# Kernel tuning notes

Measured on AMD Instinct MI355X. Metric: run time of the kernel, lower is better.

The kernel has to match this reference:

```python
import jax, jax.numpy as jnp
import numpy as np

N = 100000          # nodes
E = 1600000         # edges (avg degree 16)
H = 128             # hidden_dim
P = 10              # INVARIANT_PHYSICS_DIM
TOTAL = P + H
LN_EPS = 1e-5       # torch LayerNorm default


def setup_inputs() -> dict:
    key = jax.random.key(0)
    ks = jax.random.split(key, 16)
    s = 0.02
    return {
        "physics_x": jax.random.normal(ks[0], (N, P), dtype=jnp.float32),
        "learnable_emb": jax.random.normal(ks[1], (N, H), dtype=jnp.float32),
        "edge_index": jax.random.randint(ks[2], (2, E), 0, N, dtype=jnp.int32),
        "Wq": jax.random.normal(ks[3], (TOTAL, H), dtype=jnp.float32) * s,
        "bq": jnp.zeros((H,), dtype=jnp.float32),
        "Wk": jax.random.normal(ks[4], (TOTAL, H), dtype=jnp.float32) * s,
        "bk": jnp.zeros((H,), dtype=jnp.float32),
        "Wv": jax.random.normal(ks[5], (H, H), dtype=jnp.float32) * s,
        "bv": jnp.zeros((H,), dtype=jnp.float32),
        "Wo": jax.random.normal(ks[6], (H, H), dtype=jnp.float32) * s,
        "bo": jnp.zeros((H,), dtype=jnp.float32),
        "gamma": jnp.ones((H,), dtype=jnp.float32),
        "beta": jnp.zeros((H,), dtype=jnp.float32),
    }


def reference(physics_x, learnable_emb, edge_index, Wq, bq, Wk, bk, Wv, bv, Wo, bo, gamma, beta):
    n_nodes = learnable_emb.shape[0]
    scale = 1.0 / np.sqrt(Wq.shape[1]).astype(np.float32)

    full_repr = jnp.concatenate([physics_x, learnable_emb], axis=-1)   # [N, P+H]
    Q = full_repr @ Wq + bq                                            # [N, H]
    K = full_repr @ Wk + bk                                            # [N, H]
    V = learnable_emb @ Wv + bv                                        # [N, H]

    src, dst = edge_index[0], edge_index[1]
    # per-edge unnormalized attention (NOTE: no max-subtraction, faithful to source)
    attn_scores = jnp.sum(Q[dst] * K[src], axis=-1) * scale            # [E]
    exp_scores = jnp.exp(attn_scores)                                  # [E]
    denom = jax.ops.segment_sum(exp_scores, dst, num_segments=n_nodes) # [N]
    attn_probs = exp_scores / (denom[dst] + 1e-8)                      # [E]

    msg = V[src] * attn_probs[:, None]                                 # [E, H]
    agg = jax.ops.segment_sum(msg, dst, num_segments=n_nodes)          # [N, H]

    out = agg @ Wo + bo
    x = learnable_emb + out
    mu = jnp.mean(x, axis=-1, keepdims=True)
    var = jnp.var(x, axis=-1, keepdims=True)
    return gamma * (x - mu) / jnp.sqrt(var + LN_EPS) + beta
```

## Files before the change

kernel.cpp:

```cpp
#include <hip/hip_runtime.h>
#include <hip/hip_bf16.h>
#include <math.h>

#define PDIM 10
#define HDIM 128
#define TDIM 138
#define AROW 168
#define B_LEN (5 * 8 * 64 * 8)
#define TROW 136

#define CW_WQ 0
#define CW_WK 17664
#define CW_WV 35328
#define CW_WO 51712
#define CW_BQ 68096
#define CW_BK 68224
#define CW_BV 68352
#define CW_BO 68480
#define CW_GA 68608
#define CW_BE 68736
#define CW_TOTAL 68864

typedef short v8s __attribute__((ext_vector_type(8)));
typedef float v4f __attribute__((ext_vector_type(4)));
typedef float v2f __attribute__((ext_vector_type(2)));

#if defined(__has_builtin)
#if __has_builtin(__builtin_amdgcn_cvt_pk_f32_fp8) && __has_builtin(__builtin_amdgcn_cvt_pk_fp8_f32)
#define HAVE_FP8_CVT 1
#endif
#endif
#ifndef HAVE_FP8_CVT
#define HAVE_FP8_CVT 0
#endif

__device__ __forceinline__ float b2f_lo(unsigned u) { return __uint_as_float(u << 16); }
__device__ __forceinline__ float b2f_hi(unsigned u) { return __uint_as_float(u & 0xffff0000u); }
__device__ __forceinline__ unsigned short f2b(float f) {
    unsigned u = __float_as_uint(f);
    u += 0x7fffu + ((u >> 16) & 1u);
    return (unsigned short)(u >> 16);
}

__device__ __forceinline__ float f8_dec1(unsigned b) {
    unsigned e = (b >> 3) & 0xf, m = b & 7;
    float v = e ? __uint_as_float(((e + 120) << 23) | (m << 20))
                : (float)m * 0.001953125f;
    return (b & 0x80) ? -v : v;
}
__device__ __forceinline__ unsigned f8_enc1(float f) {
    unsigned u = __float_as_uint(f);
    unsigned s = (u >> 31) << 7;
    float a = fabsf(f);
    if (a < 0.0009765625f) return s;
    if (a < 0.015625f) {
        int m = (int)(a * 512.f + 0.5f); if (m > 7) m = 7;
        return s | (unsigned)m;
    }
    if (a >= 448.f) return s | 0x7e;
    int ex = (int)((u >> 23) & 0xff);
    unsigned mant = u & 0x7fffff;
    unsigned r = mant >> 20, rem = mant & 0xfffff;
    if (rem > 0x80000u || (rem == 0x80000u && (r & 1))) r++;
    if (r == 8) { r = 0; ex++; }
    if (ex - 127 > 8) return s | 0x7e;
    return s | (unsigned)((ex - 120) << 3) | r;
}

__device__ __forceinline__ void dot4(unsigned w, const float* q, float& p) {
#if HAVE_FP8_CVT
    v2f lo = __builtin_amdgcn_cvt_pk_f32_fp8((int)w, false);
    v2f hi = __builtin_amdgcn_cvt_pk_f32_fp8((int)w, true);
    p = fmaf(q[0], lo[0], p); p = fmaf(q[1], lo[1], p);
    p = fmaf(q[2], hi[0], p); p = fmaf(q[3], hi[1], p);
#else
    p = fmaf(q[0], f8_dec1(w & 0xff), p);
    p = fmaf(q[1], f8_dec1((w >> 8) & 0xff), p);
    p = fmaf(q[2], f8_dec1((w >> 16) & 0xff), p);
    p = fmaf(q[3], f8_dec1(w >> 24), p);
#endif
}
__device__ __forceinline__ void acc4(unsigned w, float e, float* acc) {
#if HAVE_FP8_CVT
    v2f lo = __builtin_amdgcn_cvt_pk_f32_fp8((int)w, false);
    v2f hi = __builtin_amdgcn_cvt_pk_f32_fp8((int)w, true);
    acc[0] = fmaf(e, lo[0], acc[0]); acc[1] = fmaf(e, lo[1], acc[1]);
    acc[2] = fmaf(e, hi[0], acc[2]); acc[3] = fmaf(e, hi[1], acc[3]);
#else
    acc[0] = fmaf(e, f8_dec1(w & 0xff), acc[0]);
    acc[1] = fmaf(e, f8_dec1((w >> 8) & 0xff), acc[1]);
    acc[2] = fmaf(e, f8_dec1((w >> 16) & 0xff), acc[2]);
    acc[3] = fmaf(e, f8_dec1(w >> 24), acc[3]);
#endif
}
__device__ __forceinline__ uint2 pack8(uint4 t) {
#if HAVE_FP8_CVT
    int u0 = __builtin_amdgcn_cvt_pk_fp8_f32(b2f_lo(t.x), b2f_hi(t.x), 0, false);
    u0 = __builtin_amdgcn_cvt_pk_fp8_f32(b2f_lo(t.y), b2f_hi(t.y), u0, true);
    int u1 = __builtin_amdgcn_cvt_pk_fp8_f32(b2f_lo(t.z), b2f_hi(t.z), 0, false);
    u1 = __builtin_amdgcn_cvt_pk_fp8_f32(b2f_lo(t.w), b2f_hi(t.w), u1, true);
    return make_uint2((unsigned)u0, (unsigned)u1);
#else
    unsigned u0 = f8_enc1(b2f_lo(t.x)) | (f8_enc1(b2f_hi(t.x)) << 8)
                | (f8_enc1(b2f_lo(t.y)) << 16) | (f8_enc1(b2f_hi(t.y)) << 24);
    unsigned u1 = f8_enc1(b2f_lo(t.z)) | (f8_enc1(b2f_hi(t.z)) << 8)
                | (f8_enc1(b2f_lo(t.w)) << 16) | (f8_enc1(b2f_hi(t.w)) << 24);
    return make_uint2(u0, u1);
#endif
}

__global__ void ws_sentinel_kernel(float* out, int bucket)
{
    if (threadIdx.x == 0) out[0] = ldexpf(1.f + (float)bucket / 256.f, 100);
}

__global__ __launch_bounds__(256) void convert_weights(
    const float* Wq, const float* Wk, const float* Wv, const float* Wo,
    const float* bq, const float* bk, const float* bv, const float* bo,
    const float* ga, const float* be,
    float* __restrict__ dst)
{
    int idx = blockIdx.x * 256 + threadIdx.x;
    if (idx >= CW_TOTAL) return;
    const float* src; int loc;
    if      (idx < CW_WK) { src = Wq; loc = idx - CW_WQ; }
    else if (idx < CW_WV) { src = Wk; loc = idx - CW_WK; }
    else if (idx < CW_WO) { src = Wv; loc = idx - CW_WV; }
    else if (idx < CW_BQ) { src = Wo; loc = idx - CW_WO; }
    else if (idx < CW_BK) { src = bq; loc = idx - CW_BQ; }
    else if (idx < CW_BV) { src = bk; loc = idx - CW_BK; }
    else if (idx < CW_BO) { src = bv; loc = idx - CW_BV; }
    else if (idx < CW_GA) { src = bo; loc = idx - CW_BO; }
    else if (idx < CW_BE) { src = ga; loc = idx - CW_GA; }
    else                  { src = be; loc = idx - CW_BE; }
    dst[idx] = src[loc];
}

__global__ __launch_bounds__(256) void pack_wfrag(
    const float* __restrict__ cw, unsigned short* __restrict__ wfrag)
{
    int g = blockIdx.x * 256 + threadIdx.x;
    if (g >= 3 * 5 * 8 * 64) return;
    int lane = g & 63;
    int nt   = (g >> 6) & 7;
    int mk   = g >> 9;
    int kc = mk % 5, mat = mk / 5;
    int quad = lane >> 4, l15 = lane & 15;
    int n = nt * 16 + l15;

    unsigned short* dst = wfrag + (size_t)g * 8;
    #pragma unroll
    for (int j = 0; j < 8; ++j) {
        int k = kc * 32 + quad * 8 + j;
        float v = 0.f;
        if (mat == 0)      { if (k < TDIM) v = cw[CW_WQ + k * HDIM + n]; }
        else if (mat == 1) { if (k < TDIM) v = cw[CW_WK + k * HDIM + n]; }
        else               { if (k >= PDIM && k < TDIM) v = cw[CW_WV + (k - PDIM) * HDIM + n]; }
        dst[j] = f2b(v);
    }
}

__global__ __launch_bounds__(256, 5) void qkv_mfma_kernel(
    const float* __restrict__ physics, const float* __restrict__ emb,
    const float* __restrict__ cw, const unsigned short* __restrict__ wfrag,
    unsigned short* __restrict__ Qb, unsigned char* __restrict__ K8,
    unsigned char* __restrict__ V8, int n_nodes)
{
    __shared__ __align__(16) unsigned short smem[64 * AROW];

    const int tid = threadIdx.x;
    const int nbase = blockIdx.x * 64;
    const int lane = tid & 63;
    const int w = tid >> 6;
    const int quad = lane >> 4;
    const int l15 = lane & 15;

    for (int idx = tid; idx < 64 * 5; idx += 256) {
        int r = idx / 5, p = idx - r * 5;
        int node = nbase + r;
        float v0 = 0.f, v1 = 0.f;
        if (node < n_nodes) {
            const float* ph = physics + (size_t)node * PDIM + 2 * p;
            v0 = ph[0]; v1 = ph[1];
        }
        ((unsigned*)smem)[r * 84 + p] = (unsigned)f2b(v0) | ((unsigned)f2b(v1) << 16);
    }
    for (int idx = tid; idx < 64 * 32; idx += 256) {
        int r = idx >> 5, c = idx & 31;
        int node = nbase + r;
        float4 e = make_float4(0.f, 0.f, 0.f, 0.f);
        if (node < n_nodes) e = *(const float4*)(emb + (size_t)node * HDIM + 4 * c);
        unsigned* dst = (unsigned*)smem + r * 84 + 5 + 2 * c;
        dst[0] = (unsigned)f2b(e.x) | ((unsigned)f2b(e.y) << 16);
        dst[1] = (unsigned)f2b(e.z) | ((unsigned)f2b(e.w) << 16);
    }
    for (int idx = tid; idx < 64 * 15; idx += 256) {
        int r = idx / 15, p = idx - r * 15;
        ((unsigned*)smem)[r * 84 + 69 + p] = 0;
    }
    __syncthreads();

    v8s a_frag[5];
    #pragma unroll
    for (int kc = 0; kc < 5; ++kc)
        a_frag[kc] = *(v8s*)(smem + (w * 16 + l15) * AROW + kc * 32 + quad * 8);
    __syncthreads();

    const int r_out = tid >> 2;
    const int cseg = (tid & 3) * 32;
    const int node_out = nbase + r_out;

    for (int mat = 0; mat < 3; ++mat) {
        const v8s* bglob = (const v8s*)(wfrag + (size_t)mat * B_LEN) + lane;

        v4f acc[8];
        #pragma unroll
        for (int nt = 0; nt < 8; ++nt) acc[nt] = (v4f){0.f, 0.f, 0.f, 0.f};

        #pragma unroll
        for (int kc = 0; kc < 5; ++kc) {
            #pragma unroll
            for (int nt = 0; nt < 8; ++nt) {
                v8s b = bglob[(kc * 8 + nt) * 64];
                acc[nt] = __builtin_amdgcn_mfma_f32_16x16x32_bf16(
                    a_frag[kc], b, acc[nt], 0, 0, 0);
            }
        }

        #pragma unroll
        for (int nt = 0; nt < 8; ++nt) {
            float bias = cw[CW_BQ + mat * HDIM + nt * 16 + l15];
            #pragma unroll
            for (int reg = 0; reg < 4; ++reg) {
                int row = w * 16 + quad * 4 + reg;
                smem[row * TROW + nt * 16 + l15] = f2b(acc[nt][reg] + bias);
            }
        }
        __syncthreads();

        if (node_out < n_nodes) {
            const unsigned short* srcp = smem + r_out * TROW + cseg;
            if (mat == 0) {
                unsigned short* dst = Qb + (size_t)node_out * HDIM + cseg;
                #pragma unroll
                for (int j = 0; j < 4; ++j)
                    ((uint4*)dst)[j] = *(const uint4*)(srcp + 8 * j);
            } else {
                unsigned char* dst8 = (mat == 1 ? K8 : V8) + (size_t)node_out * HDIM + cseg;
                uint4 t0 = *(const uint4*)(srcp);
                uint4 t1 = *(const uint4*)(srcp + 8);
                uint4 t2 = *(const uint4*)(srcp + 16);
                uint4 t3 = *(const uint4*)(srcp + 24);
                uint2 p0 = pack8(t0), p1 = pack8(t1), p2 = pack8(t2), p3 = pack8(t3);
                ((uint4*)dst8)[0] = make_uint4(p0.x, p0.y, p1.x, p1.y);
                ((uint4*)dst8)[1] = make_uint4(p2.x, p2.y, p3.x, p3.y);
            }
        }
        if (mat < 2) __syncthreads();
    }
}

__global__ __launch_bounds__(256) void degree_kernel(
    const int* __restrict__ ei, int* __restrict__ deg, int n_edges, int n_nodes)
{
    int e = blockIdx.x * 256 + threadIdx.x;
    if (e < n_edges) {
        int d = ei[n_edges + e];
        d = max(0, min(d, n_nodes - 1));
        atomicAdd(&deg[d], 1);
    }
}

__global__ __launch_bounds__(256) void scan_bsum(
    const int* __restrict__ deg, int* __restrict__ bsum, int n)
{
    __shared__ int s[256];
    int i = blockIdx.x * 256 + threadIdx.x;
    s[threadIdx.x] = (i < n) ? deg[i] : 0;
    __syncthreads();
    for (int off = 128; off > 0; off >>= 1) {
        if (threadIdx.x < off) s[threadIdx.x] += s[threadIdx.x + off];
        __syncthreads();
    }
    if (threadIdx.x == 0) bsum[blockIdx.x] = s[0];
}

__global__ __launch_bounds__(512) void scan_boff(
    const int* __restrict__ bsum, int* __restrict__ boff, int nb)
{
    __shared__ int s[512];
    int t = threadIdx.x;
    int v = (t < nb) ? bsum[t] : 0;
    s[t] = v;
    __syncthreads();
    for (int off = 1; off < 512; off <<= 1) {
        int u = (t >= off) ? s[t - off] : 0;
        __syncthreads();
        s[t] += u;
        __syncthreads();
    }
    if (t < nb) boff[t] = s[t] - v;
}

__global__ __launch_bounds__(256) void scan_final(
    const int* __restrict__ deg, const int* __restrict__ boff,
    int* __restrict__ row_off, int n)
{
    __shared__ int s[256];
    int t = threadIdx.x;
    int i = blockIdx.x * 256 + t;
    int v = (i < n) ? deg[i] : 0;
    s[t] = v;
    __syncthreads();
    for (int off = 1; off < 256; off <<= 1) {
        int u = (t >= off) ? s[t - off] : 0;
        __syncthreads();
        s[t] += u;
        __syncthreads();
    }
    int base = boff[blockIdx.x];
    if (i < n) row_off[i] = base + s[t] - v;
    if (i == n - 1) row_off[n] = base + s[t];
}

#define FILL_NPART 8
#define FILL_CHUNKS 512
__global__ __launch_bounds__(256) void fill_part_kernel(
    const int* __restrict__ ei, const int* __restrict__ row_off,
    int* __restrict__ cursor, int* __restrict__ csr_src, int n_edges, int n_nodes)
{
    const int part = blockIdx.x & (FILL_NPART - 1);
    const int chunk = blockIdx.x >> 3;
    const int W = (n_nodes + FILL_NPART - 1) / FILL_NPART;
    const int lo = part * W;
    const int hi = min(n_nodes, lo + W);
    const int epc = (n_edges + FILL_CHUNKS - 1) / FILL_CHUNKS;
    const int e0 = chunk * epc;
    const int e1 = min(n_edges, e0 + epc);

    for (int e = e0 + (int)threadIdx.x; e < e1; e += 256) {
        int d = ei[n_edges + e];
        d = max(0, min(d, n_nodes - 1));
        if (d >= lo && d < hi) {
            int pos = atomicAdd(&cursor[d], 1);
            csr_src[row_off[d] + pos] = ei[e];
        }
    }
}

__global__ __launch_bounds__(256) void attn_fused_kernel(
    const unsigned short* __restrict__ Qb, const unsigned char* __restrict__ K8,
    const unsigned char* __restrict__ V8,
    const int* __restrict__ row_off, const int* __restrict__ csr_src,
    float* __restrict__ agg, int n_nodes, int n_edges)
{
    const int wid = (int)((blockIdx.x * 256 + threadIdx.x) >> 6);
    const int lane = threadIdx.x & 63;
    if (wid >= n_nodes) return;
    const int eg = lane >> 3;
    const int cg = lane & 7;

    const float scale = 0.088388347648318447f;
    const uint4* qp = (const uint4*)(Qb + (size_t)wid * HDIM + cg * 16);
    uint4 qa = qp[0], qb = qp[1];
    float q[16];
    q[0]  = b2f_lo(qa.x) * scale; q[1]  = b2f_hi(qa.x) * scale;
    q[2]  = b2f_lo(qa.y) * scale; q[3]  = b2f_hi(qa.y) * scale;
    q[4]  = b2f_lo(qa.z) * scale; q[5]  = b2f_hi(qa.z) * scale;
    q[6]  = b2f_lo(qa.w) * scale; q[7]  = b2f_hi(qa.w) * scale;
    q[8]  = b2f_lo(qb.x) * scale; q[9]  = b2f_hi(qb.x) * scale;
    q[10] = b2f_lo(qb.y) * scale; q[11] = b2f_hi(qb.y) * scale;
    q[12] = b2f_lo(qb.z) * scale; q[13] = b2f_hi(qb.z) * scale;
    q[14] = b2f_lo(qb.w) * scale; q[15] = b2f_hi(qb.w) * scale;

    int beg = row_off[wid], end = row_off[wid + 1];
    beg = max(0, min(beg, n_edges));
    end = max(beg, min(end, n_edges));

    float acc[16];
    #pragma unroll
    for (int j = 0; j < 16; ++j) acc[j] = 0.f;
    float den = 0.f;

    for (int i = beg; i < end; i += 8) {
        int idx = i + eg;
        bool valid = idx < end;
        int s = csr_src[valid ? idx : (end - 1)];
        s = max(0, min(s, n_nodes - 1));
        uint4 kr = *(const uint4*)(K8 + (size_t)s * HDIM + cg * 16);
        uint4 vr = *(const uint4*)(V8 + (size_t)s * HDIM + cg * 16);

        float p = 0.f;
        dot4(kr.x, q + 0, p);
        dot4(kr.y, q + 4, p);
        dot4(kr.z, q + 8, p);
        dot4(kr.w, q + 12, p);
        p += __shfl_xor(p, 1);
        p += __shfl_xor(p, 2);
        p += __shfl_xor(p, 4);

        float e = valid ? __expf(fminf(p, 60.f)) : 0.f;
        den += e;
        acc4(vr.x, e, acc + 0);
        acc4(vr.y, e, acc + 4);
        acc4(vr.z, e, acc + 8);
        acc4(vr.w, e, acc + 12);
    }

    #pragma unroll
    for (int j = 0; j < 16; ++j) {
        acc[j] += __shfl_xor(acc[j], 8);
        acc[j] += __shfl_xor(acc[j], 16);
        acc[j] += __shfl_xor(acc[j], 32);
    }
    den += __shfl_xor(den, 8);
    den += __shfl_xor(den, 16);
    den += __shfl_xor(den, 32);

    float inv = 1.f / (den + 1e-8f);
    if (eg == 0) {
        float* dst = agg + (size_t)wid * HDIM + cg * 16;
        #pragma unroll
        for (int j = 0; j < 4; ++j)
            *(float4*)(dst + 4 * j) = make_float4(acc[4*j] * inv, acc[4*j+1] * inv,
                                                 acc[4*j+2] * inv, acc[4*j+3] * inv);
    }
}

#define LNROW 132
__global__ __launch_bounds__(256) void out_ln_kernel(
    const float* __restrict__ emb,
    const float* __restrict__ cw,
    float* __restrict__ out, int n_nodes)
{
    __shared__ float lds[32 * LNROW];
    const int tid = threadIdx.x;
    const int nbase = blockIdx.x * 32;

    for (int idx = tid; idx < 32 * 32; idx += 256) {
        int m = idx >> 5;
        int cc = idx & 31;
        int node = nbase + m;
        float4 v = make_float4(0.f, 0.f, 0.f, 0.f);
        if (node < n_nodes) v = *(const float4*)(out + (size_t)node * HDIM + 4 * cc);
        *(float4*)(lds + m * LNROW + 4 * cc) = v;
    }
    __syncthreads();

    const int c = tid & 31;
    const int g = tid >> 5;
    const float* Wo = cw + CW_WO;

    float acc[4][4] = {{0.f}};
    for (int t = 0; t < HDIM; ++t) {
        float rr[4];
        #pragma unroll
        for (int m = 0; m < 4; ++m) rr[m] = lds[(4 * g + m) * LNROW + t];
        float4 w4 = *(const float4*)(Wo + t * HDIM + 4 * c);
        float wa[4] = { w4.x, w4.y, w4.z, w4.w };
        #pragma unroll
        for (int m = 0; m < 4; ++m)
            #pragma unroll
            for (int j = 0; j < 4; ++j)
                acc[m][j] = fmaf(rr[m], wa[j], acc[m][j]);
    }

    float4 bo4 = *(const float4*)(cw + CW_BO + 4 * c);
    float4 ga4 = *(const float4*)(cw + CW_GA + 4 * c);
    float4 be4 = *(const float4*)(cw + CW_BE + 4 * c);
    float boa[4] = { bo4.x, bo4.y, bo4.z, bo4.w };
    float ga[4]  = { ga4.x, ga4.y, ga4.z, ga4.w };
    float ba[4]  = { be4.x, be4.y, be4.z, be4.w };

    #pragma unroll
    for (int m = 0; m < 4; ++m) {
        int node = nbase + 4 * g + m;
        float ea[4] = { 0.f, 0.f, 0.f, 0.f };
        if (node < n_nodes) {
            float4 e4 = *(const float4*)(emb + (size_t)node * HDIM + 4 * c);
            ea[0] = e4.x; ea[1] = e4.y; ea[2] = e4.z; ea[3] = e4.w;
        }

        float x[4], s1 = 0.f, s2 = 0.f;
        #pragma unroll
        for (int j = 0; j < 4; ++j) {
            x[j] = ea[j] + acc[m][j] + boa[j];
            s1 += x[j];
            s2 = fmaf(x[j], x[j], s2);
        }
        #pragma unroll
        for (int mask = 1; mask <= 16; mask <<= 1) {
            s1 += __shfl_xor(s1, mask);
            s2 += __shfl_xor(s2, mask);
        }
        float mu = s1 * (1.f / 128.f);
        float var = fmaxf(s2 * (1.f / 128.f) - mu * mu, 0.f);
        float rs = rsqrtf(var + 1e-5f);
        if (node < n_nodes) {
            float4 o;
            o.x = ga[0] * (x[0] - mu) * rs + ba[0];
            o.y = ga[1] * (x[1] - mu) * rs + ba[1];
            o.z = ga[2] * (x[2] - mu) * rs + ba[2];
            o.w = ga[3] * (x[3] - mu) * rs + ba[3];
            *(float4*)(out + (size_t)node * HDIM + 4 * c) = o;
        }
    }
}

extern "C" void kernel_launch(void* const* d_in, const int* in_sizes, int n_in,
                              void* d_out, int out_size, void* d_ws, size_t ws_size,
                              hipStream_t stream)
{
    const float* physics = (const float*)d_in[0];
    const float* emb     = (const float*)d_in[1];
    const int*   ei      = (const int*)d_in[2];

    const int n_nodes = in_sizes[1] / HDIM;
    const int n_edges = in_sizes[2] / 2;
    const int NB = (n_nodes + 255) / 256;

    char* ws = (char*)d_ws;
    size_t off = 0;
    auto alloc = [&](size_t bytes) -> void* {
        void* p = ws + off;
        off = (off + bytes + 255) & ~(size_t)255;
        return p;
    };

    float* cw      = (float*)alloc((size_t)CW_TOTAL * 4);
    unsigned short* wfrag = (unsigned short*)alloc((size_t)3 * B_LEN * 2);
    int* deg       = (int*)alloc((size_t)2 * n_nodes * 4);
    int* cursor    = deg + n_nodes;
    int* row_off   = (int*)alloc((size_t)(n_nodes + 1) * 4);
    int* bsum      = (int*)alloc((size_t)NB * 4);
    int* boff      = (int*)alloc((size_t)NB * 4);
    int* csr_src   = (int*)alloc((size_t)n_edges * 4);
    unsigned short* Qb = (unsigned short*)alloc((size_t)n_nodes * HDIM * 2);
    unsigned char* K8  = (unsigned char*)alloc((size_t)n_nodes * HDIM);
    unsigned char* V8  = (unsigned char*)alloc((size_t)n_nodes * HDIM);

    if (ws_size < off) {
        int bucket = (int)min((size_t)255, ws_size >> 24);
        ws_sentinel_kernel<<<1, 64, 0, stream>>>((float*)d_out, bucket);
        return;
    }

    hipMemsetAsync(deg, 0, (size_t)2 * n_nodes * sizeof(int), stream);

    convert_weights<<<(CW_TOTAL + 255) / 256, 256, 0, stream>>>(
        (const float*)d_in[3], (const float*)d_in[5], (const float*)d_in[7],
        (const float*)d_in[9], (const float*)d_in[4], (const float*)d_in[6],
        (const float*)d_in[8], (const float*)d_in[10], (const float*)d_in[11],
        (const float*)d_in[12], cw);

    pack_wfrag<<<(3 * 5 * 8 * 64 + 255) / 256, 256, 0, stream>>>(cw, wfrag);
    qkv_mfma_kernel<<<(n_nodes + 63) / 64, 256, 0, stream>>>(
        physics, emb, cw, wfrag, Qb, K8, V8, n_nodes);

    degree_kernel<<<(n_edges + 255) / 256, 256, 0, stream>>>(ei, deg, n_edges, n_nodes);
    scan_bsum<<<NB, 256, 0, stream>>>(deg, bsum, n_nodes);
    scan_boff<<<1, 512, 0, stream>>>(bsum, boff, NB);
    scan_final<<<NB, 256, 0, stream>>>(deg, boff, row_off, n_nodes);
    fill_part_kernel<<<FILL_NPART * FILL_CHUNKS, 256, 0, stream>>>(
        ei, row_off, cursor, csr_src, n_edges, n_nodes);

    attn_fused_kernel<<<(n_nodes + 3) / 4, 256, 0, stream>>>(
        Qb, K8, V8, row_off, csr_src, (float*)d_out, n_nodes, n_edges);

    out_ln_kernel<<<(n_nodes + 31) / 32, 256, 0, stream>>>(
        emb, cw, (float*)d_out, n_nodes);
}
```

Measured before the change: 457.4 us.

## Compute output projection with bf16 MFMA and store aggregation as bf16

The aggregation result is now written as bf16 to a separate workspace buffer instead of fp32 into the output. The scalar-FMA output projection plus LayerNorm kernel is replaced by one that feeds the Wo product through bf16 MFMA instructions, using a fourth pre-packed weight fragment set. LayerNorm statistics are reduced across lanes in MFMA layout. This cuts ALU time and the bytes read for agg, at the cost of bf16 rounding on agg and Wo and less coalesced per-element emb reads and output stores.

Measured after the change: 427.1 us. -6.6%, faster.

```diff
diff --git a/kernel.cpp b/kernel.cpp
--- a/kernel.cpp
+++ b/kernel.cpp
@@ -6,6 +6,7 @@
 #define HDIM 128
 #define TDIM 138
 #define AROW 168
+#define AROW2 136
 #define B_LEN (5 * 8 * 64 * 8)
 #define TROW 136
 
@@ -140,7 +141,7 @@
     const float* __restrict__ cw, unsigned short* __restrict__ wfrag)
 {
     int g = blockIdx.x * 256 + threadIdx.x;
-    if (g >= 3 * 5 * 8 * 64) return;
+    if (g >= 4 * 5 * 8 * 64) return;
     int lane = g & 63;
     int nt   = (g >> 6) & 7;
     int mk   = g >> 9;
@@ -155,7 +156,8 @@
         float v = 0.f;
         if (mat == 0)      { if (k < TDIM) v = cw[CW_WQ + k * HDIM + n]; }
         else if (mat == 1) { if (k < TDIM) v = cw[CW_WK + k * HDIM + n]; }
-        else               { if (k >= PDIM && k < TDIM) v = cw[CW_WV + (k - PDIM) * HDIM + n]; }
+        else if (mat == 2) { if (k >= PDIM && k < TDIM) v = cw[CW_WV + (k - PDIM) * HDIM + n]; }
+        else               { if (k < HDIM) v = cw[CW_WO + k * HDIM + n]; }
         dst[j] = f2b(v);
     }
 }
@@ -352,7 +354,7 @@
     const unsigned short* __restrict__ Qb, const unsigned char* __restrict__ K8,
     const unsigned char* __restrict__ V8,
     const int* __restrict__ row_off, const int* __restrict__ csr_src,
-    float* __restrict__ agg, int n_nodes, int n_edges)
+    unsigned short* __restrict__ aggb, int n_nodes, int n_edges)
 {
     const int wid = (int)((blockIdx.x * 256 + threadIdx.x) >> 6);
     const int lane = threadIdx.x & 63;
@@ -419,90 +421,105 @@
 
     float inv = 1.f / (den + 1e-8f);
     if (eg == 0) {
-        float* dst = agg + (size_t)wid * HDIM + cg * 16;
-        #pragma unroll
-        for (int j = 0; j < 4; ++j)
-            *(float4*)(dst + 4 * j) = make_float4(acc[4*j] * inv, acc[4*j+1] * inv,
-                                                 acc[4*j+2] * inv, acc[4*j+3] * inv);
-    }
-}
-
-#define LNROW 132
-__global__ __launch_bounds__(256) void out_ln_kernel(
-    const float* __restrict__ emb,
-    const float* __restrict__ cw,
+        unsigned* dst = (unsigned*)(aggb + (size_t)wid * HDIM + cg * 16);
+        #pragma unroll
+        for (int j = 0; j < 8; ++j)
+            dst[j] = (unsigned)f2b(acc[2*j] * inv)
+                   | ((unsigned)f2b(acc[2*j+1] * inv) << 16);
+    }
+}
+
+__global__ __launch_bounds__(256) void out_ln_mfma_kernel(
+    const unsigned short* __restrict__ aggb, const float* __restrict__ emb,
+    const float* __restrict__ cw, const unsigned short* __restrict__ wfrag,
     float* __restrict__ out, int n_nodes)
 {
-    __shared__ float lds[32 * LNROW];
+    __shared__ __align__(16) unsigned short smem[64 * AROW2];
     const int tid = threadIdx.x;
-    const int nbase = blockIdx.x * 32;
-
-    for (int idx = tid; idx < 32 * 32; idx += 256) {
-        int m = idx >> 5;
-        int cc = idx & 31;
-        int node = nbase + m;
-        float4 v = make_float4(0.f, 0.f, 0.f, 0.f);
-        if (node < n_nodes) v = *(const float4*)(out + (size_t)node * HDIM + 4 * cc);
-        *(float4*)(lds + m * LNROW + 4 * cc) = v;
+    const int nbase = blockIdx.x * 64;
+    const int lane = tid & 63;
+    const int w = tid >> 6;
+    const int quad = lane >> 4;
+    const int l15 = lane & 15;
+
+    for (int idx = tid; idx < 64 * 16; idx += 256) {
+        int r = idx >> 4, c = idx & 15;
+        int node = nbase + r;
+        uint4 v = make_uint4(0u, 0u, 0u, 0u);
+        if (node < n_nodes) v = ((const uint4*)(aggb + (size_t)node * HDIM))[c];
+        *(uint4*)((char*)smem + r * (AROW2 * 2) + c * 16) = v;
     }
     __syncthreads();
 
-    const int c = tid & 31;
-    const int g = tid >> 5;
-    const float* Wo = cw + CW_WO;
-
-    float acc[4][4] = {{0.f}};
-    for (int t = 0; t < HDIM; ++t) {
-        float rr[4];
-        #pragma unroll
-        for (int m = 0; m < 4; ++m) rr[m] = lds[(4 * g + m) * LNROW + t];
-        float4 w4 = *(const float4*)(Wo + t * HDIM + 4 * c);
-        float wa[4] = { w4.x, w4.y, w4.z, w4.w };
-        #pragma unroll
-        for (int m = 0; m < 4; ++m)
-            #pragma unroll
-            for (int j = 0; j < 4; ++j)
-                acc[m][j] = fmaf(rr[m], wa[j], acc[m][j]);
-    }
-
-    float4 bo4 = *(const float4*)(cw + CW_BO + 4 * c);
-    float4 ga4 = *(const float4*)(cw + CW_GA + 4 * c);
-    float4 be4 = *(const float4*)(cw + CW_BE + 4 * c);
-    float boa[4] = { bo4.x, bo4.y, bo4.z, bo4.w };
-    float ga[4]  = { ga4.x, ga4.y, ga4.z, ga4.w };
-    float ba[4]  = { be4.x, be4.y, be4.z, be4.w };
-
-    #pragma unroll
-    for (int m = 0; m < 4; ++m) {
-        int node = nbase + 4 * g + m;
-        float ea[4] = { 0.f, 0.f, 0.f, 0.f };
-        if (node < n_nodes) {
-            float4 e4 = *(const float4*)(emb + (size_t)node * HDIM + 4 * c);
-            ea[0] = e4.x; ea[1] = e4.y; ea[2] = e4.z; ea[3] = e4.w;
-        }
-
-        float x[4], s1 = 0.f, s2 = 0.f;
-        #pragma unroll
-        for (int j = 0; j < 4; ++j) {
-            x[j] = ea[j] + acc[m][j] + boa[j];
-            s1 += x[j];
-            s2 = fmaf(x[j], x[j], s2);
-        }
-        #pragma unroll
-        for (int mask = 1; mask <= 16; mask <<= 1) {
-            s1 += __shfl_xor(s1, mask);
-            s2 += __shfl_xor(s2, mask);
-        }
-        float mu = s1 * (1.f / 128.f);
-        float var = fmaxf(s2 * (1.f / 128.f) - mu * mu, 0.f);
-        float rs = rsqrtf(var + 1e-5f);
-        if (node < n_nodes) {
-            float4 o;
-            o.x = ga[0] * (x[0] - mu) * rs + ba[0];
-            o.y = ga[1] * (x[1] - mu) * rs + ba[1];
-            o.z = ga[2] * (x[2] - mu) * rs + ba[2];
-            o.w = ga[3] * (x[3] - mu) * rs + ba[3];
-            *(float4*)(out + (size_t)node * HDIM + 4 * c) = o;
+    v8s a_frag[4];
+    #pragma unroll
+    for (int kc = 0; kc < 4; ++kc)
+        a_frag[kc] = *(v8s*)(smem + (w * 16 + l15) * AROW2 + kc * 32 + quad * 8);
+
+    const v8s* bglob = (const v8s*)(wfrag + (size_t)3 * B_LEN) + lane;
+    v4f acc[8];
+    #pragma unroll
+    for (int nt = 0; nt < 8; ++nt) acc[nt] = (v4f){0.f, 0.f, 0.f, 0.f};
+
+    #pragma unroll
+    for (int kc = 0; kc < 4; ++kc) {
+        #pragma unroll
+        for (int nt = 0; nt < 8; ++nt) {
+            v8s b = bglob[(kc * 8 + nt) * 64];
+            acc[nt] = __builtin_amdgcn_mfma_f32_16x16x32_bf16(
+                a_frag[kc], b, acc[nt], 0, 0, 0);
+        }
+    }
+
+    const int row = w * 16 + quad * 4;
+    #pragma unroll
+    for (int nt = 0; nt < 8; ++nt) {
+        int col = nt * 16 + l15;
+        float bo_v = cw[CW_BO + col];
+        #pragma unroll
+        for (int reg = 0; reg < 4; ++reg) {
+            int node = nbase + row + reg;
+            float e = (node < n_nodes) ? emb[(size_t)node * HDIM + col] : 0.f;
+            acc[nt][reg] += bo_v + e;
+        }
+    }
+
+    float s1[4] = {0.f, 0.f, 0.f, 0.f};
+    float s2[4] = {0.f, 0.f, 0.f, 0.f};
+    #pragma unroll
+    for (int nt = 0; nt < 8; ++nt)
+        #pragma unroll
+        for (int reg = 0; reg < 4; ++reg) {
+            s1[reg] += acc[nt][reg];
+            s2[reg] = fmaf(acc[nt][reg], acc[nt][reg], s2[reg]);
+        }
+    #pragma unroll
+    for (int mask = 1; mask <= 8; mask <<= 1) {
+        #pragma unroll
+        for (int reg = 0; reg < 4; ++reg) {
+            s1[reg] += __shfl_xor(s1[reg], mask);
+            s2[reg] += __shfl_xor(s2[reg], mask);
+        }
+    }
+    float mu[4], rs[4];
+    #pragma unroll
+    for (int reg = 0; reg < 4; ++reg) {
+        mu[reg] = s1[reg] * (1.f / 128.f);
+        float var = fmaxf(s2[reg] * (1.f / 128.f) - mu[reg] * mu[reg], 0.f);
+        rs[reg] = rsqrtf(var + 1e-5f);
+    }
+
+    #pragma unroll
+    for (int nt = 0; nt < 8; ++nt) {
+        int col = nt * 16 + l15;
+        float ga_v = cw[CW_GA + col];
+        float be_v = cw[CW_BE + col];
+        #pragma unroll
+        for (int reg = 0; reg < 4; ++reg) {
+            int node = nbase + row + reg;
+            if (node < n_nodes)
+                out[(size_t)node * HDIM + col] =
+                    ga_v * (acc[nt][reg] - mu[reg]) * rs[reg] + be_v;
         }
     }
 }
@@ -528,7 +545,7 @@
     };
 
     float* cw      = (float*)alloc((size_t)CW_TOTAL * 4);
-    unsigned short* wfrag = (unsigned short*)alloc((size_t)3 * B_LEN * 2);
+    unsigned short* wfrag = (unsigned short*)alloc((size_t)4 * B_LEN * 2);
     int* deg       = (int*)alloc((size_t)2 * n_nodes * 4);
     int* cursor    = deg + n_nodes;
     int* row_off   = (int*)alloc((size_t)(n_nodes + 1) * 4);
@@ -538,6 +555,7 @@
     unsigned short* Qb = (unsigned short*)alloc((size_t)n_nodes * HDIM * 2);
     unsigned char* K8  = (unsigned char*)alloc((size_t)n_nodes * HDIM);
     unsigned char* V8  = (unsigned char*)alloc((size_t)n_nodes * HDIM);
+    unsigned short* aggb = (unsigned short*)alloc((size_t)n_nodes * HDIM * 2);
 
     if (ws_size < off) {
         int bucket = (int)min((size_t)255, ws_size >> 24);
@@ -553,7 +571,7 @@
         (const float*)d_in[8], (const float*)d_in[10], (const float*)d_in[11],
         (const float*)d_in[12], cw);
 
-    pack_wfrag<<<(3 * 5 * 8 * 64 + 255) / 256, 256, 0, stream>>>(cw, wfrag);
+    pack_wfrag<<<(4 * 5 * 8 * 64 + 255) / 256, 256, 0, stream>>>(cw, wfrag);
     qkv_mfma_kernel<<<(n_nodes + 63) / 64, 256, 0, stream>>>(
         physics, emb, cw, wfrag, Qb, K8, V8, n_nodes);
 
@@ -565,8 +583,8 @@
         ei, row_off, cursor, csr_src, n_edges, n_nodes);
 
     attn_fused_kernel<<<(n_nodes + 3) / 4, 256, 0, stream>>>(
-        Qb, K8, V8, row_off, csr_src, (float*)d_out, n_nodes, n_edges);
-
-    out_ln_kernel<<<(n_nodes + 31) / 32, 256, 0, stream>>>(
-        emb, cw, (float*)d_out, n_nodes);
-}
+        Qb, K8, V8, row_off, csr_src, aggb, n_nodes, n_edges);
+
+    out_ln_mfma_kernel<<<(n_nodes + 63) / 64, 256, 0, stream>>>(
+        aggb, emb, cw, wfrag, (float*)d_out, n_nodes);
+}
```
